# Kernel optimization log

Hardware: AMD Instinct MI355X
Metric: run time of the kernel (lower is better)

The kernel has to match this reference:

```python
import jax, jax.numpy as jnp
import numpy as np

C_IN, D_MODEL, TAO, M = 7, 512, 3, 5
KERNELS = D_MODEL // C_IN              # 73
LEFTOUT = D_MODEL - C_IN * KERNELS     # 1
B, L = 32, 4096


def setup_inputs() -> dict:
    key = jax.random.key(0)
    k1, k2, k3, k4, k5 = jax.random.split(key, 5)
    x = jax.random.normal(k1, (B, L, C_IN), dtype=jnp.float32)
    # kaiming_normal fan_in, leaky_relu (negative_slope=0.01): gain^2/fan_in
    fan_in = (M + 1) * 3
    std = float(np.sqrt(2.0 / (fan_in * (1.0 + 0.01 ** 2))))
    conv_w = jax.random.normal(k2, (KERNELS, M + 1, 3), dtype=jnp.float32) * std
    bound = float(1.0 / np.sqrt(fan_in))
    conv_b = jax.random.uniform(k3, (KERNELS,), jnp.float32, -bound, bound)
    leftout_w = jax.random.uniform(k4, (LEFTOUT, M + 1, 3), jnp.float32, -bound, bound)
    leftout_b = jax.random.uniform(k5, (LEFTOUT,), jnp.float32, -bound, bound)
    return {"x": x, "conv_w": conv_w, "conv_b": conv_b,
            "leftout_w": leftout_w, "leftout_b": leftout_b}


def _circ_conv1d(inp, w, b):
    # inp: [N, Cin, L]; w: [Cout, Cin, 3]; circular padding of 1 on each side
    xp = jnp.concatenate([inp[..., -1:], inp, inp[..., :1]], axis=-1)
    y = jax.lax.conv_general_dilated(xp, w, window_strides=(1,), padding='VALID',
                                     dimension_numbers=('NCH', 'OIH', 'NCH'))
    return y + b[None, :, None]


def reference(x, conv_w, conv_b, leftout_w, leftout_b):
    b, n, c = x.shape  # [B, L, C_IN]
    # delay-coordinate embedding: emb[b, t, c, i] = x[b, t - i*tao, c], zero for t < m*tao
    idx = jnp.arange(n)[:, None] - jnp.arange(M + 1)[None, :] * TAO   # [L, m+1]
    g = x[:, jnp.clip(idx, 0, n - 1), :]                              # [B, L, m+1, C]
    valid = (jnp.arange(n) >= M * TAO)[None, :, None, None]
    g = jnp.where(valid, g, jnp.zeros((), x.dtype))
    # chunk j (over channels) is [B, m+1, L]; all share the same conv -> batch over B*C
    chunks = jnp.transpose(g, (0, 3, 2, 1))                           # [B, C, m+1, L]
    flat = chunks.reshape(b * c, M + 1, n)
    y = _circ_conv1d(flat, conv_w, conv_b).reshape(b, c * KERNELS, n)  # [B, C*K, L]
    y_left = _circ_conv1d(chunks[:, -1], leftout_w, leftout_b)         # [B, LEFTOUT, L]
    out = jnp.concatenate([y, y_left], axis=1)                         # [B, D_MODEL, L]
    return jnp.transpose(out, (0, 2, 1))                               # [B, L, D_MODEL]
```

## Files before the change

### kernel.cpp

```cpp
#include <hip/hip_runtime.h>

#define C_IN     7
#define D_MODEL  512
#define TAO      3
#define M_TAPS   5
#define KERNELS  73
#define B_SZ     32
#define L_SZ     4096
#define TB       64
#define NTB      (L_SZ / TB)
#define ROWS     (TB + 17)
#define RPAD     84
#define CHUNK    8
#define NCHUNK   (TB / CHUNK)

__global__ __launch_bounds__(512, 4) void trc_conv_kernel(
    const float* __restrict__ x,
    const float* __restrict__ conv_w,
    const float* __restrict__ conv_b,
    const float* __restrict__ leftout_w,
    const float* __restrict__ leftout_b,
    float* __restrict__ out)
{
    __shared__ float xs[C_IN][RPAD];
    __shared__ __align__(16) float buf[2][CHUNK][D_MODEL];

    const int tid = threadIdx.x;
    const int b   = blockIdx.x / NTB;
    const int tb  = blockIdx.x % NTB;
    const int t0  = tb * TB;

    const float* xb = x + (size_t)b * L_SZ * C_IN;
    for (int i = tid; i < ROWS * C_IN; i += 512) {
        int r = i / C_IN, c = i - r * C_IN;
        int g = t0 - 16 + r;
        if (g < 0)      g += L_SZ;
        if (g >= L_SZ)  g -= L_SZ;
        xs[c][r] = xb[(size_t)g * C_IN + c];
    }
    __syncthreads();

    const int d = tid;
    int ch;
    const float* wsrc;
    float bias;
    if (d < C_IN * KERNELS) {
        ch = d / KERNELS;
        int o = d - ch * KERNELS;
        wsrc = conv_w + o * 18;
        bias = conv_b[o];
    } else {
        ch = C_IN - 1;
        wsrc = leftout_w;
        bias = leftout_b[0];
    }
    const float* __restrict__ row = &xs[ch][0];

    float wreg[18];
    #pragma unroll
    for (int j = 0; j < 18; ++j) {
        int k = j % 3;
        int m = (15 + k - j) / 3;
        wreg[j] = wsrc[m * 3 + k];
    }

    const bool first = (tb == 0), last = (tb == NTB - 1);
    float4* outv = (float4*)(out + ((size_t)b * L_SZ + t0) * D_MODEL);

    float win[18];
    #pragma unroll
    for (int j = 0; j < 17; ++j) win[j] = row[j];

    #pragma unroll
    for (int c = 0; c < NCHUNK; ++c) {
        #pragma unroll
        for (int i = 0; i < CHUNK; ++i) {
            const int tl = c * CHUNK + i;
            win[(tl + 17) % 18] = row[tl + 17];
            float acc = bias;
            if ((first && tl < 16) || (last && tl == TB - 1)) {
                #pragma unroll
                for (int k = 0; k < 3; ++k) {
                    int tt = t0 + tl + k - 1;
                    if (tt < 0)      tt += L_SZ;
                    if (tt >= L_SZ)  tt -= L_SZ;
                    if (tt >= M_TAPS * TAO) {
                        int lt = tl + 15 + k;
                        #pragma unroll
                        for (int m = 0; m < 6; ++m)
                            acc = fmaf(row[lt - 3 * m], wreg[15 + k - 3 * m], acc);
                    }
                }
            } else {
                #pragma unroll
                for (int j = 0; j < 18; ++j)
                    acc = fmaf(win[(tl + j) % 18], wreg[j], acc);
            }
            buf[c & 1][i][d] = acc;
        }
        __builtin_amdgcn_sched_barrier(0);
        asm volatile("s_waitcnt lgkmcnt(0)" ::: "memory");
        __builtin_amdgcn_sched_barrier(0);
        __builtin_amdgcn_s_barrier();
        __builtin_amdgcn_sched_barrier(0);

        const float4* bv = (const float4*)&buf[c & 1][0][0];
        float4 v0 = bv[tid];
        float4 v1 = bv[tid + 512];
        outv[c * 1024 + tid]       = v0;
        outv[c * 1024 + tid + 512] = v1;
    }
}

extern "C" void kernel_launch(void* const* d_in, const int* in_sizes, int n_in,
                              void* d_out, int out_size, void* d_ws, size_t ws_size,
                              hipStream_t stream) {
    const float* x          = (const float*)d_in[0];
    const float* conv_w     = (const float*)d_in[1];
    const float* conv_b     = (const float*)d_in[2];
    const float* leftout_w  = (const float*)d_in[3];
    const float* leftout_b  = (const float*)d_in[4];
    float* out = (float*)d_out;

    dim3 grid(B_SZ * NTB);
    trc_conv_kernel<<<grid, 512, 0, stream>>>(x, conv_w, conv_b,
                                              leftout_w, leftout_b, out);
}
```

Baseline: 51.52 us.

## Halve time tile, stage whole tile in LDS, store once after single barrier

```diff
diff --git a/kernel.cpp b/kernel.cpp
--- a/kernel.cpp
+++ b/kernel.cpp
@@ -7,14 +7,14 @@
 #define KERNELS  73
 #define B_SZ     32
 #define L_SZ     4096
-#define TB       64
+#define TB       32
 #define NTB      (L_SZ / TB)
 #define ROWS     (TB + 17)
-#define RPAD     84
+#define RPAD     52
 #define CHUNK    8
-#define NCHUNK   (TB / CHUNK)
+#define NCH      (TB / CHUNK)
 
-__global__ __launch_bounds__(512, 4) void trc_conv_kernel(
+__global__ __launch_bounds__(512, 2) void trc_conv_kernel(
     const float* __restrict__ x,
     const float* __restrict__ conv_w,
     const float* __restrict__ conv_b,
@@ -23,7 +23,7 @@
     float* __restrict__ out)
 {
     __shared__ float xs[C_IN][RPAD];
-    __shared__ __align__(16) float buf[2][CHUNK][D_MODEL];
+    __shared__ __align__(16) float buf[TB][D_MODEL];
 
     const int tid = threadIdx.x;
     const int b   = blockIdx.x / NTB;
@@ -31,8 +31,8 @@
     const int t0  = tb * TB;
 
     const float* xb = x + (size_t)b * L_SZ * C_IN;
-    for (int i = tid; i < ROWS * C_IN; i += 512) {
-        int r = i / C_IN, c = i - r * C_IN;
+    if (tid < ROWS * C_IN) {
+        int r = tid / C_IN, c = tid - r * C_IN;
         int g = t0 - 16 + r;
         if (g < 0)      g += L_SZ;
         if (g >= L_SZ)  g -= L_SZ;
@@ -64,52 +64,69 @@
         wreg[j] = wsrc[m * 3 + k];
     }
 
-    const bool first = (tb == 0), last = (tb == NTB - 1);
-    float4* outv = (float4*)(out + ((size_t)b * L_SZ + t0) * D_MODEL);
+    if (tb == 0 || tb == NTB - 1) {
+        for (int tl = 0; tl < TB; ++tl) {
+            float acc = bias;
+            #pragma unroll
+            for (int k = 0; k < 3; ++k) {
+                int tt = t0 + tl + k - 1;
+                if (tt < 0)      tt += L_SZ;
+                if (tt >= L_SZ)  tt -= L_SZ;
+                if (tt >= M_TAPS * TAO) {
+                    int lt = tl + 15 + k;
+                    #pragma unroll
+                    for (int m = 0; m < 6; ++m)
+                        acc = fmaf(row[lt - 3 * m], wreg[15 + k - 3 * m], acc);
+                }
+            }
+            buf[tl][d] = acc;
+        }
+    } else {
+        float win[25];
+        #pragma unroll
+        for (int q = 0; q < 17; ++q) win[q] = row[q];
 
-    float win[18];
-    #pragma unroll
-    for (int j = 0; j < 17; ++j) win[j] = row[j];
-
-    #pragma unroll
-    for (int c = 0; c < NCHUNK; ++c) {
-        #pragma unroll
-        for (int i = 0; i < CHUNK; ++i) {
-            const int tl = c * CHUNK + i;
-            win[(tl + 17) % 18] = row[tl + 17];
-            float acc = bias;
-            if ((first && tl < 16) || (last && tl == TB - 1)) {
-                #pragma unroll
-                for (int k = 0; k < 3; ++k) {
-                    int tt = t0 + tl + k - 1;
-                    if (tt < 0)      tt += L_SZ;
-                    if (tt >= L_SZ)  tt -= L_SZ;
-                    if (tt >= M_TAPS * TAO) {
-                        int lt = tl + 15 + k;
-                        #pragma unroll
-                        for (int m = 0; m < 6; ++m)
-                            acc = fmaf(row[lt - 3 * m], wreg[15 + k - 3 * m], acc);
-                    }
-                }
-            } else {
+        for (int c = 0; c < NCH; ++c) {
+            #pragma unroll
+            for (int i = 0; i < CHUNK; ++i) win[17 + i] = row[c * CHUNK + 17 + i];
+            #pragma unroll
+            for (int i = 0; i < CHUNK; ++i) {
+                float acc = bias;
                 #pragma unroll
                 for (int j = 0; j < 18; ++j)
-                    acc = fmaf(win[(tl + j) % 18], wreg[j], acc);
+                    acc = fmaf(win[i + j], wreg[j], acc);
+                buf[c * CHUNK + i][d] = acc;
             }
-            buf[c & 1][i][d] = acc;
+            #pragma unroll
+            for (int q = 0; q < 17; ++q) win[q] = win[q + CHUNK];
         }
-        __builtin_amdgcn_sched_barrier(0);
-        asm volatile("s_waitcnt lgkmcnt(0)" ::: "memory");
-        __builtin_amdgcn_sched_barrier(0);
-        __builtin_amdgcn_s_barrier();
-        __builtin_amdgcn_sched_barrier(0);
+    }
 
-        const float4* bv = (const float4*)&buf[c & 1][0][0];
-        float4 v0 = bv[tid];
-        float4 v1 = bv[tid + 512];
-        outv[c * 1024 + tid]       = v0;
-        outv[c * 1024 + tid + 512] = v1;
-    }
+    __builtin_amdgcn_sched_barrier(0);
+    asm volatile("s_waitcnt lgkmcnt(0)" ::: "memory");
+    __builtin_amdgcn_sched_barrier(0);
+    __builtin_amdgcn_s_barrier();
+    __builtin_amdgcn_sched_barrier(0);
+
+    const float4* bv = (const float4*)&buf[0][0];
+    float4 v0 = bv[tid];
+    float4 v1 = bv[tid + 512];
+    float4 v2 = bv[tid + 1024];
+    float4 v3 = bv[tid + 1536];
+    float4 v4 = bv[tid + 2048];
+    float4 v5 = bv[tid + 2560];
+    float4 v6 = bv[tid + 3072];
+    float4 v7 = bv[tid + 3584];
+
+    float4* o4 = (float4*)(out + ((size_t)b * L_SZ + t0) * D_MODEL);
+    o4[tid]        = v0;
+    o4[tid + 512]  = v1;
+    o4[tid + 1024] = v2;
+    o4[tid + 1536] = v3;
+    o4[tid + 2048] = v4;
+    o4[tid + 2560] = v5;
+    o4[tid + 3072] = v6;
+    o4[tid + 3584] = v7;
 }
 
 extern "C" void kernel_launch(void* const* d_in, const int* in_sizes, int n_in,
```

Result: slower. 66.81 us (+29.7%).
